# Optimization experiments

Hardware: AMD Instinct MI355X
Metric: run time of the kernel (lower is better)

## Reference

```python
import math
import jax, jax.numpy as jnp
from jax import lax
import numpy as np

E = 16        # num experts
K = 2         # top_k
CF = 1.25     # capacity factor


def setup_inputs() -> dict:
    key = jax.random.key(0)
    k0, k1, k2, k3, k4 = jax.random.split(key, 5)
    B, S, D, H = 2, 2048, 1024, 1024
    scale = 0.02
    return {
        "x": jax.random.normal(k0, (B, S, D), dtype=jnp.float32),
        "router_w": jax.random.normal(k1, (D, E), dtype=jnp.float32) * scale,
        "gate_w": jax.random.normal(k2, (E, D, H), dtype=jnp.float32) * scale,
        "up_w": jax.random.normal(k3, (E, D, H), dtype=jnp.float32) * scale,
        "down_w": jax.random.normal(k4, (E, H, D), dtype=jnp.float32) * scale,
    }


def reference(x, router_w, gate_w, up_w, down_w):
    B, S, D = x.shape
    xf = x.reshape(-1, D)                     # [T, D]
    T = B * S
    capacity = max(1, math.ceil(T * K / E * CF))   # static python int
    Cbuf = K * capacity                       # per-expert buffer (per-column capacity x K)

    # ---- router: softmax over experts, then top-k (weights = top-k probs) ----
    logits = xf @ router_w                    # [T, E]
    probs = jax.nn.softmax(logits, axis=-1)
    w, idx = lax.top_k(probs, K)              # [T, K] each

    # ---- capacity drop: per k-column, per expert, keep first `capacity` tokens ----
    oh = jax.nn.one_hot(idx, E, dtype=w.dtype)            # [T, K, E]
    rank = jnp.cumsum(oh, axis=0) - oh                     # exclusive rank per (k, e)
    myrank = jnp.sum(rank * oh, axis=-1)                   # [T, K]
    keep = myrank < capacity
    w = jnp.where(keep, w, 0.0)

    # ---- dispatch: scatter kept assignments into [E, Cbuf] slots ----
    flat_e = idx.reshape(-1)                               # [A], A = T*K (row-major: token-major)
    flat_w = w.reshape(-1)
    keep_f = keep.reshape(-1)
    tok = jnp.repeat(jnp.arange(T, dtype=jnp.int32), K)    # [A]
    ohk = jax.nn.one_hot(flat_e, E, dtype=jnp.int32) * keep_f[:, None].astype(jnp.int32)
    pos = jnp.cumsum(ohk, axis=0) - ohk                    # exclusive rank among kept per expert
    slot = jnp.sum(pos * ohk, axis=-1)                     # [A], < Cbuf for kept
    e_idx = jnp.where(keep_f, flat_e, E)                   # dropped -> dummy expert row E

    dispatch = jnp.full((E + 1, Cbuf), T, dtype=jnp.int32).at[e_idx, slot].set(tok)
    wbuf = jnp.zeros((E + 1, Cbuf), dtype=w.dtype).at[e_idx, slot].set(flat_w)
    dispatch = dispatch[:E]
    wbuf = wbuf[:E]

    x_pad = jnp.concatenate([xf, jnp.zeros((1, D), xf.dtype)], axis=0)  # sentinel row
    xe = x_pad[dispatch]                                   # [E, Cbuf, D]

    # ---- grouped SwiGLU expert GEMMs ----
    gate = jnp.einsum('ecd,edh->ech', xe, gate_w)
    up = jnp.einsum('ecd,edh->ech', xe, up_w)
    hidden = jax.nn.silu(gate) * up
    out = jnp.einsum('ech,ehd->ecd', hidden, down_w)       # [E, Cbuf, D]
    out = out * wbuf[:, :, None]

    # ---- combine: scatter-add back to tokens ----
    combined = jnp.zeros((T + 1, D), dtype=xf.dtype).at[dispatch.reshape(-1)].add(out.reshape(-1, D))
    return combined[:T].reshape(B, S, D)
```

## Files before the change

kernel.cpp:

```cpp
#include <hip/hip_runtime.h>
#include <math.h>

#define T_TOK 4096
#define DIM   1024
#define HID   1024
#define NE    16
#define CAP   640
#define CBUF  1280
#define BM 128
#define BN 64
#define BK 32
#define MAXTILE 160

typedef __attribute__((ext_vector_type(8))) short short8;
typedef __attribute__((ext_vector_type(4))) float f32x4;

static __device__ __forceinline__ unsigned short f2bf(float f) {
    unsigned int u = __float_as_uint(f);
    u += 0x7fff + ((u >> 16) & 1);
    return (unsigned short)(u >> 16);
}

static __device__ __forceinline__ void async16(const void* g, void* l) {
    __builtin_amdgcn_global_load_lds((const __attribute__((address_space(1))) void*)g,
                                     (__attribute__((address_space(3))) void*)l, 16, 0, 0);
}

__global__ void convert_x_k(const float* __restrict__ x, unsigned short* __restrict__ xb) {
    int i = blockIdx.x * blockDim.x + threadIdx.x;
    int base = i * 4;
    int row = base >> 10;
    ushort4 o;
    if (row < T_TOK) {
        float4 v = *(const float4*)(x + base);
        o.x = f2bf(v.x); o.y = f2bf(v.y); o.z = f2bf(v.z); o.w = f2bf(v.w);
    } else {
        o.x = 0; o.y = 0; o.z = 0; o.w = 0;
    }
    *(ushort4*)(xb + base) = o;
}

#define TK 512
#define TN 32
__global__ __launch_bounds__(256)
void transpose_cvt_k(const float* __restrict__ W0, const float* __restrict__ W1,
                     const float* __restrict__ W2,
                     unsigned short* __restrict__ T0, unsigned short* __restrict__ T1,
                     unsigned short* __restrict__ T2) {
    __shared__ unsigned short s[TN * TK];
    int zz = blockIdx.z;
    int which = zz >> 4, e = zz & 15;
    const float* W = (which == 0) ? W0 : (which == 1) ? W1 : W2;
    unsigned short* T = (which == 0) ? T0 : (which == 1) ? T1 : T2;
    const float* Wp = W + (size_t)e * DIM * HID;
    unsigned short* Tp = T + (size_t)e * DIM * HID;
    int k0 = blockIdx.y * TK, n0 = blockIdx.x * TN;
    int tid = threadIdx.x;

    int tx = tid & 7, ty = tid >> 3;
    const float* src = Wp + (size_t)(k0 + ty) * 1024 + n0 + tx * 4;
    #pragma unroll
    for (int sw = 0; sw < 16; ++sw) {
        float4 v = *(const float4*)(src + (size_t)sw * 32 * 1024);
        int kk = sw * 32 + ty;
        int kks = kk ^ (tx << 3);
        float vv[4] = {v.x, v.y, v.z, v.w};
        #pragma unroll
        for (int i = 0; i < 4; ++i) {
            int n = tx * 4 + i;
            s[n * TK + kks] = f2bf(vv[i]);
        }
    }
    __syncthreads();

    int wv = tid >> 6, lane = tid & 63;
    #pragma unroll
    for (int r = 0; r < 8; ++r) {
        int n = wv * 8 + r;
        int swz = (n >> 2) & 7;
        uint4 o = *(const uint4*)&s[n * TK + ((lane ^ swz) << 3)];
        *(uint4*)(Tp + (size_t)(n0 + n) * 1024 + k0 + lane * 8) = o;
    }
}

__global__ void router_k(const float* __restrict__ x, const float* __restrict__ rw,
                         int* __restrict__ route_e, float* __restrict__ route_w) {
    int t = blockIdx.x;
    int lane = threadIdx.x;
    const float* xr = x + (size_t)t * DIM + lane * 16;
    float4 xv0 = *(const float4*)(xr + 0);
    float4 xv1 = *(const float4*)(xr + 4);
    float4 xv2 = *(const float4*)(xr + 8);
    float4 xv3 = *(const float4*)(xr + 12);
    float xl[16] = {xv0.x, xv0.y, xv0.z, xv0.w, xv1.x, xv1.y, xv1.z, xv1.w,
                    xv2.x, xv2.y, xv2.z, xv2.w, xv3.x, xv3.y, xv3.z, xv3.w};
    float p[16];
    #pragma unroll
    for (int e = 0; e < 16; ++e) p[e] = 0.f;
    #pragma unroll
    for (int j = 0; j < 16; ++j) {
        const float4* rp = (const float4*)(rw + (size_t)(lane * 16 + j) * 16);
        float4 r0 = rp[0], r1 = rp[1], r2 = rp[2], r3 = rp[3];
        float xv = xl[j];
        p[0]  += xv * r0.x; p[1]  += xv * r0.y; p[2]  += xv * r0.z; p[3]  += xv * r0.w;
        p[4]  += xv * r1.x; p[5]  += xv * r1.y; p[6]  += xv * r1.z; p[7]  += xv * r1.w;
        p[8]  += xv * r2.x; p[9]  += xv * r2.y; p[10] += xv * r2.z; p[11] += xv * r2.w;
        p[12] += xv * r3.x; p[13] += xv * r3.y; p[14] += xv * r3.z; p[15] += xv * r3.w;
    }
    #pragma unroll
    for (int off = 32; off > 0; off >>= 1) {
        #pragma unroll
        for (int e = 0; e < 16; ++e) p[e] += __shfl_xor(p[e], off);
    }
    if (lane == 0) {
        float m = p[0];
        #pragma unroll
        for (int e = 1; e < 16; ++e) m = fmaxf(m, p[e]);
        float s = 0.f;
        #pragma unroll
        for (int e = 0; e < 16; ++e) s = s + __expf(p[e] - m);
        float v0 = -1e30f, v1 = -1e30f; int i0 = 0, i1 = 0;
        #pragma unroll
        for (int e = 0; e < 16; ++e) {
            float v = p[e];
            if (v > v0)      { v1 = v0; i1 = i0; v0 = v; i0 = e; }
            else if (v > v1) { v1 = v;  i1 = e; }
        }
        route_e[t*2+0] = i0;  route_e[t*2+1] = i1;
        route_w[t*2+0] = __expf(v0 - m) / s;
        route_w[t*2+1] = __expf(v1 - m) / s;
    }
}

__global__ __launch_bounds__(1024)
void build_dispatch_k(const int* __restrict__ route_e, const float* __restrict__ route_w,
                      int* __restrict__ disp, int* __restrict__ smap, int* __restrict__ tmeta) {
    __shared__ unsigned char eidx[2 * T_TOK];
    __shared__ unsigned char keepf[2 * T_TOK];
    __shared__ int totals[NE];
    int tid = threadIdx.x;
    int wv = tid >> 6, lane = tid & 63;

    {
        int4 a = ((const int4*)route_e)[tid * 2];
        int4 b = ((const int4*)route_e)[tid * 2 + 1];
        unsigned int lo = (a.x & 0xff) | ((a.y & 0xff) << 8) | ((a.z & 0xff) << 16) | ((a.w & 0xff) << 24);
        unsigned int hi = (b.x & 0xff) | ((b.y & 0xff) << 8) | ((b.z & 0xff) << 16) | ((b.w & 0xff) << 24);
        uint2 pk; pk.x = lo; pk.y = hi;
        *(uint2*)(eidx + tid * 8) = pk;
    }
    for (int i = tid; i < 2 * T_TOK; i += 1024) smap[i] = -1;
    __syncthreads();

    unsigned long long below = (lane == 0) ? 0ull : ((~0ull) >> (64 - lane));
    #pragma unroll
    for (int s = 0; s < 2; ++s) {
        int st = wv + s * 16;
        int e = st >> 1, k = st & 1;
        int run = 0;
        for (int base = 0; base < T_TOK; base += 64) {
            int t = base + lane;
            int hit = (eidx[t * 2 + k] == e);
            unsigned long long m = __ballot(hit);
            int rank = run + __popcll(m & below);
            if (hit) keepf[t * 2 + k] = (rank < CAP) ? 1 : 0;
            run += __popcll(m);
        }
    }
    __syncthreads();

    {
        int e = wv;
        int run = 0;
        for (int base = 0; base < 2 * T_TOK; base += 64) {
            int f = base + lane;
            int hit = (eidx[f] == e) && keepf[f];
            unsigned long long m = __ballot(hit);
            int slot = run + __popcll(m & below);
            if (hit) {
                disp[e * CBUF + slot] = f >> 1;
                smap[f] = e * CBUF + slot;
            }
            run += __popcll(m);
        }
        if (lane == 0) totals[e] = run;
    }
    __syncthreads();

    for (int i = tid; i < NE * CBUF; i += 1024) {
        int e = i / CBUF, s = i - e * CBUF;
        if (s >= totals[e]) disp[i] = T_TOK;
    }

    if (tid == 0) {
        int n = 0;
        for (int e = 0; e < NE; ++e) {
            int ntl = (totals[e] + BM - 1) / BM;
            for (int m = 0; m < ntl; ++m) { tmeta[4 + n] = (e << 8) | m; ++n; }
        }
        tmeta[0] = n;
    }
}

__global__ __launch_bounds__(256, 2)
void gemm1_k(const unsigned short* __restrict__ xb, const unsigned short* __restrict__ gt,
             const unsigned short* __restrict__ ut, const int* __restrict__ disp,
             const int* __restrict__ tmeta, unsigned short* __restrict__ hidden) {
    int slot = blockIdx.y;
    if (slot >= tmeta[0]) return;
    int pk = tmeta[4 + slot];
    int e = pk >> 8, mt = pk & 255;
    int m0 = mt * BM, n0 = blockIdx.x * BN;

    __shared__ unsigned short As[2 * BM * BK];
    __shared__ unsigned short Bg[2 * BN * BK];
    __shared__ unsigned short Bu[2 * BN * BK];
    __shared__ int tok[BM];
    int tid = threadIdx.x;
    if (tid < BM) tok[tid] = disp[e * CBUF + m0 + tid];
    __syncthreads();

    int lane = tid & 63, w = tid >> 6;
    int cg = (lane & 3) ^ ((lane >> 3) & 3);
    int rl = lane >> 2;
    int rA0 = w * 32 + rl, rA1 = rA0 + 16;
    const unsigned short* srcA0 = xb + (size_t)tok[rA0] * DIM + cg * 8;
    const unsigned short* srcA1 = xb + (size_t)tok[rA1] * DIM + cg * 8;
    const unsigned short* srcG  = gt + ((size_t)e * HID + n0 + w * 16 + rl) * DIM + cg * 8;
    const unsigned short* srcU  = ut + ((size_t)e * HID + n0 + w * 16 + rl) * DIM + cg * 8;
    unsigned short* dA0 = As + (w * 32) * BK;
    unsigned short* dA1 = As + (w * 32 + 16) * BK;
    unsigned short* dG  = Bg + (w * 16) * BK;
    unsigned short* dU  = Bu + (w * 16) * BK;

    int wm = w >> 1, wn = w & 1;
    int quad = lane >> 4, ln = lane & 15;
    int swq = quad ^ ((ln >> 1) & 3);

    f32x4 zero4 = {0.f, 0.f, 0.f, 0.f};
    f32x4 accg[4][2], accu[4][2];
    #pragma unroll
    for (int i = 0; i < 4; ++i)
        #pragma unroll
        for (int j = 0; j < 2; ++j) { accg[i][j] = zero4; accu[i][j] = zero4; }

    async16(srcA0, dA0); async16(srcA1, dA1);
    async16(srcG, dG);   async16(srcU, dU);

    for (int k0 = 0; k0 < DIM; k0 += BK) {
        int cur = (k0 >> 5) & 1;
        asm volatile("s_waitcnt vmcnt(0)\n\ts_barrier" ::: "memory");
        if (k0 + BK < DIM) {
            int nx = cur ^ 1, nk = k0 + BK;
            async16(srcA0 + nk, dA0 + nx * (BM * BK));
            async16(srcA1 + nk, dA1 + nx * (BM * BK));
            async16(srcG + nk,  dG + nx * (BN * BK));
            async16(srcU + nk,  dU + nx * (BN * BK));
        }
        const unsigned short* Ab = As + cur * (BM * BK);
        const unsigned short* Gb = Bg + cur * (BN * BK);
        const unsigned short* Ub = Bu + cur * (BN * BK);
        short8 af[4], bgf[2], buf2[2];
        #pragma unroll
        for (int i = 0; i < 4; ++i)
            af[i] = *(const short8*)(Ab + (wm * 64 + i * 16 + ln) * BK + swq * 8);
        #pragma unroll
        for (int j = 0; j < 2; ++j) {
            bgf[j]  = *(const short8*)(Gb + (wn * 32 + j * 16 + ln) * BK + swq * 8);
            buf2[j] = *(const short8*)(Ub + (wn * 32 + j * 16 + ln) * BK + swq * 8);
        }
        #pragma unroll
        for (int i = 0; i < 4; ++i)
            #pragma unroll
            for (int j = 0; j < 2; ++j) {
                accg[i][j] = __builtin_amdgcn_mfma_f32_16x16x32_bf16(af[i], bgf[j],  accg[i][j], 0, 0, 0);
                accu[i][j] = __builtin_amdgcn_mfma_f32_16x16x32_bf16(af[i], buf2[j], accu[i][j], 0, 0, 0);
            }
    }
    #pragma unroll
    for (int i = 0; i < 4; ++i) {
        #pragma unroll
        for (int r = 0; r < 4; ++r) {
            int row = m0 + wm * 64 + i * 16 + quad * 4 + r;
            unsigned short* hrow = hidden + ((size_t)e * CBUF + row) * HID + n0 + wn * 32 + ln;
            #pragma unroll
            for (int j = 0; j < 2; ++j) {
                float g = accg[i][j][r];
                float u = accu[i][j][r];
                float sg = g / (1.f + __expf(-g));
                hrow[j * 16] = f2bf(sg * u);
            }
        }
    }
}

__global__ __launch_bounds__(256, 2)
void gemm2_k(const unsigned short* __restrict__ hidden, const unsigned short* __restrict__ dt,
             const int* __restrict__ tmeta, unsigned short* __restrict__ ebuf) {
    int slot = blockIdx.y;
    if (slot >= tmeta[0]) return;
    int pk = tmeta[4 + slot];
    int e = pk >> 8, mt = pk & 255;
    int m0 = mt * BM, n0 = blockIdx.x * BN;

    __shared__ unsigned short As[2 * BM * BK];
    __shared__ unsigned short Bs[2 * BN * BK];
    int tid = threadIdx.x;

    int lane = tid & 63, w = tid >> 6;
    int cg = (lane & 3) ^ ((lane >> 3) & 3);
    int rl = lane >> 2;
    int rA0 = w * 32 + rl, rA1 = rA0 + 16;
    const unsigned short* srcA0 = hidden + ((size_t)e * CBUF + m0 + rA0) * HID + cg * 8;
    const unsigned short* srcA1 = hidden + ((size_t)e * CBUF + m0 + rA1) * HID + cg * 8;
    const unsigned short* srcB  = dt + ((size_t)e * DIM + n0 + w * 16 + rl) * HID + cg * 8;
    unsigned short* dA0 = As + (w * 32) * BK;
    unsigned short* dA1 = As + (w * 32 + 16) * BK;
    unsigned short* dB  = Bs + (w * 16) * BK;

    int wm = w >> 1, wn = w & 1;
    int quad = lane >> 4, ln = lane & 15;
    int swq = quad ^ ((ln >> 1) & 3);

    f32x4 zero4 = {0.f, 0.f, 0.f, 0.f};
    f32x4 acc[4][2];
    #pragma unroll
    for (int i = 0; i < 4; ++i)
        #pragma unroll
        for (int j = 0; j < 2; ++j) acc[i][j] = zero4;

    async16(srcA0, dA0); async16(srcA1, dA1);
    async16(srcB, dB);

    for (int k0 = 0; k0 < HID; k0 += BK) {
        int cur = (k0 >> 5) & 1;
        asm volatile("s_waitcnt vmcnt(0)\n\ts_barrier" ::: "memory");
        if (k0 + BK < HID) {
            int nx = cur ^ 1, nk = k0 + BK;
            async16(srcA0 + nk, dA0 + nx * (BM * BK));
            async16(srcA1 + nk, dA1 + nx * (BM * BK));
            async16(srcB + nk,  dB + nx * (BN * BK));
        }
        const unsigned short* Ab = As + cur * (BM * BK);
        const unsigned short* Bb = Bs + cur * (BN * BK);
        short8 af[4], bf[2];
        #pragma unroll
        for (int i = 0; i < 4; ++i)
            af[i] = *(const short8*)(Ab + (wm * 64 + i * 16 + ln) * BK + swq * 8);
        #pragma unroll
        for (int j = 0; j < 2; ++j)
            bf[j] = *(const short8*)(Bb + (wn * 32 + j * 16 + ln) * BK + swq * 8);
        #pragma unroll
        for (int i = 0; i < 4; ++i)
            #pragma unroll
            for (int j = 0; j < 2; ++j)
                acc[i][j] = __builtin_amdgcn_mfma_f32_16x16x32_bf16(af[i], bf[j], acc[i][j], 0, 0, 0);
    }
    #pragma unroll
    for (int i = 0; i < 4; ++i) {
        #pragma unroll
        for (int r = 0; r < 4; ++r) {
            int row = m0 + wm * 64 + i * 16 + quad * 4 + r;
            unsigned short* erow = ebuf + ((size_t)e * CBUF + row) * DIM + n0 + wn * 32 + ln;
            #pragma unroll
            for (int j = 0; j < 2; ++j)
                erow[j * 16] = f2bf(acc[i][j][r]);
        }
    }
}

__global__ __launch_bounds__(256)
void combine_k(const unsigned short* __restrict__ ebuf, const int* __restrict__ smap,
               const float* __restrict__ rwt, float* __restrict__ out) {
    int t = blockIdx.x * 2 + (threadIdx.x >> 7);
    int c = (threadIdx.x & 127) * 8;
    float acc[8];
    #pragma unroll
    for (int j = 0; j < 8; ++j) acc[j] = 0.f;
    #pragma unroll
    for (int k = 0; k < 2; ++k) {
        int sm = smap[t * 2 + k];
        if (sm >= 0) {
            float wgt = rwt[t * 2 + k];
            uint4 rv = *(const uint4*)(ebuf + (size_t)sm * DIM + c);
            unsigned int d[4] = {rv.x, rv.y, rv.z, rv.w};
            #pragma unroll
            for (int q = 0; q < 4; ++q) {
                acc[q * 2 + 0] += wgt * __uint_as_float(d[q] << 16);
                acc[q * 2 + 1] += wgt * __uint_as_float(d[q] & 0xffff0000u);
            }
        }
    }
    float4 o0 = {acc[0], acc[1], acc[2], acc[3]};
    float4 o1 = {acc[4], acc[5], acc[6], acc[7]};
    float* orow = out + (size_t)t * DIM + c;
    *(float4*)(orow + 0) = o0;
    *(float4*)(orow + 4) = o1;
}

extern "C" void kernel_launch(void* const* d_in, const int* in_sizes, int n_in,
                              void* d_out, int out_size, void* d_ws, size_t ws_size,
                              hipStream_t stream) {
    const float* x  = (const float*)d_in[0];
    const float* rw = (const float*)d_in[1];
    const float* gw = (const float*)d_in[2];
    const float* uw = (const float*)d_in[3];
    const float* dw = (const float*)d_in[4];
    float* out = (float*)d_out;

    char* ws = (char*)d_ws;
    size_t off = 0;
    auto alloc = [&](size_t bytes) { void* p = ws + off; off += (bytes + 255) & ~(size_t)255; return p; };
    unsigned short* xb  = (unsigned short*)alloc((size_t)(T_TOK + 1) * DIM * 2);
    unsigned short* gt  = (unsigned short*)alloc((size_t)NE * DIM * HID * 2);
    unsigned short* ut  = (unsigned short*)alloc((size_t)NE * DIM * HID * 2);
    unsigned short* dtw = (unsigned short*)alloc((size_t)NE * DIM * HID * 2);
    unsigned short* hid = (unsigned short*)alloc((size_t)NE * CBUF * HID * 2);
    int*   disp   = (int*)alloc((size_t)NE * CBUF * 4);
    int*   smap   = (int*)alloc((size_t)T_TOK * 2 * 4);
    int*   tmeta  = (int*)alloc((4 + MAXTILE) * 4);
    int*   re     = (int*)alloc((size_t)T_TOK * 2 * 4);
    float* rwt    = (float*)alloc((size_t)T_TOK * 2 * 4);
    unsigned short* ebuf = gt;
    (void)ws_size; (void)in_sizes; (void)n_in;

    convert_x_k<<<T_TOK + 1, 256, 0, stream>>>(x, xb);
    transpose_cvt_k<<<dim3(32, 2, 48), 256, 0, stream>>>(gw, uw, dw, gt, ut, dtw);
    router_k<<<T_TOK, 64, 0, stream>>>(x, rw, re, rwt);
    build_dispatch_k<<<1, 1024, 0, stream>>>(re, rwt, disp, smap, tmeta);
    gemm1_k<<<dim3(HID / BN, MAXTILE), 256, 0, stream>>>(xb, gt, ut, disp, tmeta, hid);
    gemm2_k<<<dim3(DIM / BN, MAXTILE), 256, 0, stream>>>(hid, dtw, tmeta, ebuf);
    combine_k<<<T_TOK / 2, 256, 0, stream>>>(ebuf, smap, rwt, out);
}
```

Before: 413.3 us.

## Fuse fp32-to-bf16 weight conversion into expert GEMM B-tile loads

Removes the standalone transpose/convert kernel that turned all gate, up and down weights into transposed bf16 copies. Both expert GEMMs now read the fp32 weights directly into registers, convert them to bf16 and store them into a new LDS swizzle, with the loads issued before the MFMA work and the LDS stores done after it. The goal is to drop the full-weight read/write pass and its launch. In exchange, every M-tile of an expert re-reads the fp32 weights at twice the bytes, relying on cache reuse, and B-tile loading moves from async global-to-LDS copies to register staging. The ebuf buffer now gets its own allocation instead of aliasing the old transposed-weight buffer.

```diff
diff --git a/kernel.cpp b/kernel.cpp
--- a/kernel.cpp
+++ b/kernel.cpp
@@ -21,6 +21,8 @@
     return (unsigned short)(u >> 16);
 }
 
+#define PICK4(v,i) ((i)==0?(v).x:(i)==1?(v).y:(i)==2?(v).z:(v).w)
+
 static __device__ __forceinline__ void async16(const void* g, void* l) {
     __builtin_amdgcn_global_load_lds((const __attribute__((address_space(1))) void*)g,
                                      (__attribute__((address_space(3))) void*)l, 16, 0, 0);
@@ -38,49 +40,6 @@
         o.x = 0; o.y = 0; o.z = 0; o.w = 0;
     }
     *(ushort4*)(xb + base) = o;
-}
-
-#define TK 512
-#define TN 32
-__global__ __launch_bounds__(256)
-void transpose_cvt_k(const float* __restrict__ W0, const float* __restrict__ W1,
-                     const float* __restrict__ W2,
-                     unsigned short* __restrict__ T0, unsigned short* __restrict__ T1,
-                     unsigned short* __restrict__ T2) {
-    __shared__ unsigned short s[TN * TK];
-    int zz = blockIdx.z;
-    int which = zz >> 4, e = zz & 15;
-    const float* W = (which == 0) ? W0 : (which == 1) ? W1 : W2;
-    unsigned short* T = (which == 0) ? T0 : (which == 1) ? T1 : T2;
-    const float* Wp = W + (size_t)e * DIM * HID;
-    unsigned short* Tp = T + (size_t)e * DIM * HID;
-    int k0 = blockIdx.y * TK, n0 = blockIdx.x * TN;
-    int tid = threadIdx.x;
-
-    int tx = tid & 7, ty = tid >> 3;
-    const float* src = Wp + (size_t)(k0 + ty) * 1024 + n0 + tx * 4;
-    #pragma unroll
-    for (int sw = 0; sw < 16; ++sw) {
-        float4 v = *(const float4*)(src + (size_t)sw * 32 * 1024);
-        int kk = sw * 32 + ty;
-        int kks = kk ^ (tx << 3);
-        float vv[4] = {v.x, v.y, v.z, v.w};
-        #pragma unroll
-        for (int i = 0; i < 4; ++i) {
-            int n = tx * 4 + i;
-            s[n * TK + kks] = f2bf(vv[i]);
-        }
-    }
-    __syncthreads();
-
-    int wv = tid >> 6, lane = tid & 63;
-    #pragma unroll
-    for (int r = 0; r < 8; ++r) {
-        int n = wv * 8 + r;
-        int swz = (n >> 2) & 7;
-        uint4 o = *(const uint4*)&s[n * TK + ((lane ^ swz) << 3)];
-        *(uint4*)(Tp + (size_t)(n0 + n) * 1024 + k0 + lane * 8) = o;
-    }
 }
 
 __global__ void router_k(const float* __restrict__ x, const float* __restrict__ rw,
@@ -203,8 +162,8 @@
 }
 
 __global__ __launch_bounds__(256, 2)
-void gemm1_k(const unsigned short* __restrict__ xb, const unsigned short* __restrict__ gt,
-             const unsigned short* __restrict__ ut, const int* __restrict__ disp,
+void gemm1_k(const unsigned short* __restrict__ xb, const float* __restrict__ gw,
+             const float* __restrict__ uw, const int* __restrict__ disp,
              const int* __restrict__ tmeta, unsigned short* __restrict__ hidden) {
     int slot = blockIdx.y;
     if (slot >= tmeta[0]) return;
@@ -226,16 +185,21 @@
     int rA0 = w * 32 + rl, rA1 = rA0 + 16;
     const unsigned short* srcA0 = xb + (size_t)tok[rA0] * DIM + cg * 8;
     const unsigned short* srcA1 = xb + (size_t)tok[rA1] * DIM + cg * 8;
-    const unsigned short* srcG  = gt + ((size_t)e * HID + n0 + w * 16 + rl) * DIM + cg * 8;
-    const unsigned short* srcU  = ut + ((size_t)e * HID + n0 + w * 16 + rl) * DIM + cg * 8;
     unsigned short* dA0 = As + (w * 32) * BK;
     unsigned short* dA1 = As + (w * 32 + 16) * BK;
-    unsigned short* dG  = Bg + (w * 16) * BK;
-    unsigned short* dU  = Bu + (w * 16) * BK;
+
+    int matb = tid >> 7;
+    int kidx = (tid >> 4) & 7;
+    int k4 = kidx * 4;
+    int g = tid & 15;
+    const float* Wsrc = (matb ? uw : gw) + (size_t)e * DIM * HID + (size_t)k4 * HID + n0 + g * 4;
+    unsigned short* Bmine = matb ? Bu : Bg;
+    int bOff = (((k4 >> 3) ^ (g & 3)) << 3) + ((k4 >> 2) & 1) * 4;
 
     int wm = w >> 1, wn = w & 1;
     int quad = lane >> 4, ln = lane & 15;
-    int swq = quad ^ ((ln >> 1) & 3);
+    int swqA = quad ^ ((ln >> 1) & 3);
+    int swqB = quad ^ ((ln >> 2) & 3);
 
     f32x4 zero4 = {0.f, 0.f, 0.f, 0.f};
     f32x4 accg[4][2], accu[4][2];
@@ -244,18 +208,33 @@
         #pragma unroll
         for (int j = 0; j < 2; ++j) { accg[i][j] = zero4; accu[i][j] = zero4; }
 
-    async16(srcA0, dA0); async16(srcA1, dA1);
-    async16(srcG, dG);   async16(srcU, dU);
+    {
+        float4 r0 = *(const float4*)(Wsrc);
+        float4 r1 = *(const float4*)(Wsrc + 1024);
+        float4 r2 = *(const float4*)(Wsrc + 2048);
+        float4 r3 = *(const float4*)(Wsrc + 3072);
+        async16(srcA0, dA0); async16(srcA1, dA1);
+        #pragma unroll
+        for (int i = 0; i < 4; ++i) {
+            uint2 pkv;
+            pkv.x = (unsigned int)f2bf(PICK4(r0, i)) | ((unsigned int)f2bf(PICK4(r1, i)) << 16);
+            pkv.y = (unsigned int)f2bf(PICK4(r2, i)) | ((unsigned int)f2bf(PICK4(r3, i)) << 16);
+            *(uint2*)(Bmine + (g * 4 + i) * BK + bOff) = pkv;
+        }
+        asm volatile("s_waitcnt vmcnt(0) lgkmcnt(0)\n\ts_barrier" ::: "memory");
+    }
 
     for (int k0 = 0; k0 < DIM; k0 += BK) {
-        int cur = (k0 >> 5) & 1;
-        asm volatile("s_waitcnt vmcnt(0)\n\ts_barrier" ::: "memory");
+        int cur = (k0 >> 5) & 1, nx = cur ^ 1;
+        float4 r0, r1, r2, r3;
         if (k0 + BK < DIM) {
-            int nx = cur ^ 1, nk = k0 + BK;
-            async16(srcA0 + nk, dA0 + nx * (BM * BK));
-            async16(srcA1 + nk, dA1 + nx * (BM * BK));
-            async16(srcG + nk,  dG + nx * (BN * BK));
-            async16(srcU + nk,  dU + nx * (BN * BK));
+            const float* Ws = Wsrc + (size_t)(k0 + BK) * 1024;
+            r0 = *(const float4*)(Ws);
+            r1 = *(const float4*)(Ws + 1024);
+            r2 = *(const float4*)(Ws + 2048);
+            r3 = *(const float4*)(Ws + 3072);
+            async16(srcA0 + k0 + BK, dA0 + nx * (BM * BK));
+            async16(srcA1 + k0 + BK, dA1 + nx * (BM * BK));
         }
         const unsigned short* Ab = As + cur * (BM * BK);
         const unsigned short* Gb = Bg + cur * (BN * BK);
@@ -263,11 +242,11 @@
         short8 af[4], bgf[2], buf2[2];
         #pragma unroll
         for (int i = 0; i < 4; ++i)
-            af[i] = *(const short8*)(Ab + (wm * 64 + i * 16 + ln) * BK + swq * 8);
+            af[i] = *(const short8*)(Ab + (wm * 64 + i * 16 + ln) * BK + swqA * 8);
         #pragma unroll
         for (int j = 0; j < 2; ++j) {
-            bgf[j]  = *(const short8*)(Gb + (wn * 32 + j * 16 + ln) * BK + swq * 8);
-            buf2[j] = *(const short8*)(Ub + (wn * 32 + j * 16 + ln) * BK + swq * 8);
+            bgf[j]  = *(const short8*)(Gb + (wn * 32 + j * 16 + ln) * BK + swqB * 8);
+            buf2[j] = *(const short8*)(Ub + (wn * 32 + j * 16 + ln) * BK + swqB * 8);
         }
         #pragma unroll
         for (int i = 0; i < 4; ++i)
@@ -276,6 +255,16 @@
                 accg[i][j] = __builtin_amdgcn_mfma_f32_16x16x32_bf16(af[i], bgf[j],  accg[i][j], 0, 0, 0);
                 accu[i][j] = __builtin_amdgcn_mfma_f32_16x16x32_bf16(af[i], buf2[j], accu[i][j], 0, 0, 0);
             }
+        if (k0 + BK < DIM) {
+            #pragma unroll
+            for (int i = 0; i < 4; ++i) {
+                uint2 pkv;
+                pkv.x = (unsigned int)f2bf(PICK4(r0, i)) | ((unsigned int)f2bf(PICK4(r1, i)) << 16);
+                pkv.y = (unsigned int)f2bf(PICK4(r2, i)) | ((unsigned int)f2bf(PICK4(r3, i)) << 16);
+                *(uint2*)(Bmine + nx * (BN * BK) + (g * 4 + i) * BK + bOff) = pkv;
+            }
+        }
+        asm volatile("s_waitcnt vmcnt(0) lgkmcnt(0)\n\ts_barrier" ::: "memory");
     }
     #pragma unroll
     for (int i = 0; i < 4; ++i) {
@@ -285,17 +274,17 @@
             unsigned short* hrow = hidden + ((size_t)e * CBUF + row) * HID + n0 + wn * 32 + ln;
             #pragma unroll
             for (int j = 0; j < 2; ++j) {
-                float g = accg[i][j][r];
-                float u = accu[i][j][r];
-                float sg = g / (1.f + __expf(-g));
-                hrow[j * 16] = f2bf(sg * u);
+                float gv = accg[i][j][r];
+                float uv = accu[i][j][r];
+                float sg = gv / (1.f + __expf(-gv));
+                hrow[j * 16] = f2bf(sg * uv);
             }
         }
     }
 }
 
 __global__ __launch_bounds__(256, 2)
-void gemm2_k(const unsigned short* __restrict__ hidden, const unsigned short* __restrict__ dt,
+void gemm2_k(const unsigned short* __restrict__ hidden, const float* __restrict__ dw,
              const int* __restrict__ tmeta, unsigned short* __restrict__ ebuf) {
     int slot = blockIdx.y;
     if (slot >= tmeta[0]) return;
@@ -313,14 +302,19 @@
     int rA0 = w * 32 + rl, rA1 = rA0 + 16;
     const unsigned short* srcA0 = hidden + ((size_t)e * CBUF + m0 + rA0) * HID + cg * 8;
     const unsigned short* srcA1 = hidden + ((size_t)e * CBUF + m0 + rA1) * HID + cg * 8;
-    const unsigned short* srcB  = dt + ((size_t)e * DIM + n0 + w * 16 + rl) * HID + cg * 8;
     unsigned short* dA0 = As + (w * 32) * BK;
     unsigned short* dA1 = As + (w * 32 + 16) * BK;
-    unsigned short* dB  = Bs + (w * 16) * BK;
+
+    int g2 = tid & 31;
+    int kidx2 = ((tid >> 5) & 3) | ((tid >> 7) << 2);
+    int k4 = kidx2 * 4;
+    const float* Wsrc = dw + (size_t)e * HID * DIM + (size_t)k4 * DIM + n0 + g2 * 2;
+    int bOff = (((k4 >> 3) ^ ((g2 >> 1) & 3)) << 3) + ((k4 >> 2) & 1) * 4;
 
     int wm = w >> 1, wn = w & 1;
     int quad = lane >> 4, ln = lane & 15;
-    int swq = quad ^ ((ln >> 1) & 3);
+    int swqA = quad ^ ((ln >> 1) & 3);
+    int swqB = quad ^ ((ln >> 2) & 3);
 
     f32x4 zero4 = {0.f, 0.f, 0.f, 0.f};
     f32x4 acc[4][2];
@@ -329,32 +323,58 @@
         #pragma unroll
         for (int j = 0; j < 2; ++j) acc[i][j] = zero4;
 
-    async16(srcA0, dA0); async16(srcA1, dA1);
-    async16(srcB, dB);
+    {
+        float2 r0 = *(const float2*)(Wsrc);
+        float2 r1 = *(const float2*)(Wsrc + 1024);
+        float2 r2 = *(const float2*)(Wsrc + 2048);
+        float2 r3 = *(const float2*)(Wsrc + 3072);
+        async16(srcA0, dA0); async16(srcA1, dA1);
+        #pragma unroll
+        for (int i = 0; i < 2; ++i) {
+            uint2 pkv;
+            pkv.x = (unsigned int)f2bf(i ? r0.y : r0.x) | ((unsigned int)f2bf(i ? r1.y : r1.x) << 16);
+            pkv.y = (unsigned int)f2bf(i ? r2.y : r2.x) | ((unsigned int)f2bf(i ? r3.y : r3.x) << 16);
+            *(uint2*)(Bs + (g2 * 2 + i) * BK + bOff) = pkv;
+        }
+        asm volatile("s_waitcnt vmcnt(0) lgkmcnt(0)\n\ts_barrier" ::: "memory");
+    }
 
     for (int k0 = 0; k0 < HID; k0 += BK) {
-        int cur = (k0 >> 5) & 1;
-        asm volatile("s_waitcnt vmcnt(0)\n\ts_barrier" ::: "memory");
+        int cur = (k0 >> 5) & 1, nx = cur ^ 1;
+        float2 r0, r1, r2, r3;
         if (k0 + BK < HID) {
-            int nx = cur ^ 1, nk = k0 + BK;
-            async16(srcA0 + nk, dA0 + nx * (BM * BK));
-            async16(srcA1 + nk, dA1 + nx * (BM * BK));
-            async16(srcB + nk,  dB + nx * (BN * BK));
+            const float* Ws = Wsrc + (size_t)(k0 + BK) * 1024;
+            r0 = *(const float2*)(Ws);
+            r1 = *(const float2*)(Ws + 1024);
+            r2 = *(const float2*)(Ws + 2048);
+            r3 = *(const float2*)(Ws + 3072);
+            async16(srcA0 + k0 + BK, dA0 + nx * (BM * BK));
+            async16(srcA1 + k0 + BK, dA1 + nx * (BM * BK));
         }
         const unsigned short* Ab = As + cur * (BM * BK);
         const unsigned short* Bb = Bs + cur * (BN * BK);
         short8 af[4], bf[2];
         #pragma unroll
         for (int i = 0; i < 4; ++i)
-            af[i] = *(const short8*)(Ab + (wm * 64 + i * 16 + ln) * BK + swq * 8);
+            af[i] = *(const short8*)(Ab + (wm * 64 + i * 16 + ln) * BK + swqA * 8);
         #pragma unroll
         for (int j = 0; j < 2; ++j)
-            bf[j] = *(const short8*)(Bb + (wn * 32 + j * 16 + ln) * BK + swq * 8);
+            bf[j] = *(const short8*)(Bb + (wn * 32 + j * 16 + ln) * BK + swqB * 8);
         #pragma unroll
         for (int i = 0; i < 4; ++i)
             #pragma unroll
             for (int j = 0; j < 2; ++j)
                 acc[i][j] = __builtin_amdgcn_mfma_f32_16x16x32_bf16(af[i], bf[j], acc[i][j], 0, 0, 0);
+        if (k0 + BK < HID) {
+            #pragma unroll
+            for (int i = 0; i < 2; ++i) {
+                uint2 pkv;
+                pkv.x = (unsigned int)f2bf(i ? r0.y : r0.x) | ((unsigned int)f2bf(i ? r1.y : r1.x) << 16);
+                pkv.y = (unsigned int)f2bf(i ? r2.y : r2.x) | ((unsigned int)f2bf(i ? r3.y : r3.x) << 16);
+                *(uint2*)(Bs + nx * (BN * BK) + (g2 * 2 + i) * BK + bOff) = pkv;
+            }
+        }
+        asm volatile("s_waitcnt vmcnt(0) lgkmcnt(0)\n\ts_barrier" ::: "memory");
     }
     #pragma unroll
     for (int i = 0; i < 4; ++i) {
@@ -411,24 +431,20 @@
     char* ws = (char*)d_ws;
     size_t off = 0;
     auto alloc = [&](size_t bytes) { void* p = ws + off; off += (bytes + 255) & ~(size_t)255; return p; };
-    unsigned short* xb  = (unsigned short*)alloc((size_t)(T_TOK + 1) * DIM * 2);
-    unsigned short* gt  = (unsigned short*)alloc((size_t)NE * DIM * HID * 2);
-    unsigned short* ut  = (unsigned short*)alloc((size_t)NE * DIM * HID * 2);
-    unsigned short* dtw = (unsigned short*)alloc((size_t)NE * DIM * HID * 2);
-    unsigned short* hid = (unsigned short*)alloc((size_t)NE * CBUF * HID * 2);
+    unsigned short* xb   = (unsigned short*)alloc((size_t)(T_TOK + 1) * DIM * 2);
+    unsigned short* hid  = (unsigned short*)alloc((size_t)NE * CBUF * HID * 2);
+    unsigned short* ebuf = (unsigned short*)alloc((size_t)NE * CBUF * DIM * 2);
     int*   disp   = (int*)alloc((size_t)NE * CBUF * 4);
     int*   smap   = (int*)alloc((size_t)T_TOK * 2 * 4);
     int*   tmeta  = (int*)alloc((4 + MAXTILE) * 4);
     int*   re     = (int*)alloc((size_t)T_TOK * 2 * 4);
     float* rwt    = (float*)alloc((size_t)T_TOK * 2 * 4);
-    unsigned short* ebuf = gt;
     (void)ws_size; (void)in_sizes; (void)n_in;
 
     convert_x_k<<<T_TOK + 1, 256, 0, stream>>>(x, xb);
-    transpose_cvt_k<<<dim3(32, 2, 48), 256, 0, stream>>>(gw, uw, dw, gt, ut, dtw);
     router_k<<<T_TOK, 64, 0, stream>>>(x, rw, re, rwt);
     build_dispatch_k<<<1, 1024, 0, stream>>>(re, rwt, disp, smap, tmeta);
-    gemm1_k<<<dim3(HID / BN, MAXTILE), 256, 0, stream>>>(xb, gt, ut, disp, tmeta, hid);
-    gemm2_k<<<dim3(DIM / BN, MAXTILE), 256, 0, stream>>>(hid, dtw, tmeta, ebuf);
+    gemm1_k<<<dim3(HID / BN, MAXTILE), 256, 0, stream>>>(xb, gw, uw, disp, tmeta, hid);
+    gemm2_k<<<dim3(DIM / BN, MAXTILE), 256, 0, stream>>>(hid, dw, tmeta, ebuf);
     combine_k<<<T_TOK / 2, 256, 0, stream>>>(ebuf, smap, rwt, out);
 }
```

After: 419.8 us. About the same (+1.6%).
